# Performance work log

Hardware: AMD Instinct MI355X
Metric: run time of the kernel (lower is better)

## Reference

```python
import jax, jax.numpy as jnp
import numpy as np

B, L, D, H, SPD = 16, 512, 768, 12, 5
DH = D // H
LN_EPS = 1e-5
CLAMP_MIN = 1e-6


def setup_inputs() -> dict:
    key = jax.random.key(0)
    ks = jax.random.split(key, 8)
    s = 1.0 / np.sqrt(D)
    return {
        "tgt": jax.random.normal(ks[0], (B, L, D), jnp.float32),
        "query_pos": jax.random.normal(ks[1], (B, L, D), jnp.float32),
        "pairwise_locs": jax.random.normal(ks[2], (B, L, L, SPD), jnp.float32),
        "Wq": jax.random.normal(ks[3], (D, D), jnp.float32) * s,
        "bq": jnp.zeros((D,), jnp.float32),
        "Wk": jax.random.normal(ks[4], (D, D), jnp.float32) * s,
        "bk": jnp.zeros((D,), jnp.float32),
        "Wv": jax.random.normal(ks[5], (D, D), jnp.float32) * s,
        "bv": jnp.zeros((D,), jnp.float32),
        "Wo": jax.random.normal(ks[6], (D, D), jnp.float32) * s,
        "bo": jnp.zeros((D,), jnp.float32),
        "Wloc": jax.random.normal(ks[7], (SPD, H), jnp.float32) * (1.0 / np.sqrt(SPD)),
        "bloc": jnp.zeros((H,), jnp.float32),
        "ln_g": jnp.ones((D,), jnp.float32),
        "ln_b": jnp.zeros((D,), jnp.float32),
    }


def _layer_norm(x, g, b):
    mu = jnp.mean(x, axis=-1, keepdims=True)
    var = jnp.mean(jnp.square(x - mu), axis=-1, keepdims=True)
    return g * (x - mu) * jax.lax.rsqrt(var + LN_EPS) + b


def reference(tgt, query_pos, pairwise_locs, Wq, bq, Wk, bk, Wv, bv, Wo, bo, Wloc, bloc, ln_g, ln_b):
    # forward_post path: q = k = tgt + query_pos; v = tgt
    qk_in = tgt + query_pos
    q = (qk_in @ Wq + bq).reshape(B, L, H, DH)   # [B,L,H,DH]
    k = (qk_in @ Wk + bk).reshape(B, L, H, DH)
    v = (tgt @ Wv + bv).reshape(B, L, H, DH)

    scale = np.float32(1.0 / np.sqrt(DH))
    attn = jnp.einsum('blhd,bthd->bhlt', q, k) * scale   # [B,H,L,L]

    # spatial fusion 'mul': relu(Linear(pairwise_locs)) -> log-domain additive bias
    loc_attn = jax.nn.relu(pairwise_locs @ Wloc + bloc)   # [B,L,L,H]
    loc_attn = jnp.transpose(loc_attn, (0, 3, 1, 2))      # [B,H,L,L]
    fused = jax.nn.softmax(jnp.log(jnp.clip(loc_attn, CLAMP_MIN, None)) + attn, axis=-1)

    out = jnp.einsum('bhlt,bthd->blhd', fused, v).reshape(B, L, D)
    out = out @ Wo + bo                                   # attn output (tgt2)

    # residual + (dropout p=0) + LayerNorm
    return _layer_norm(tgt + out, ln_g, ln_b)
```

## Files before the change

### kernel.cpp

```cpp
#include <hip/hip_runtime.h>
#include <math.h>

#define BB 16
#define LL 512
#define DD 768
#define HH 12
#define DHH 64
#define SPDD 5
#define MM (BB*LL)
#define LN_EPS 1e-5f
#define CLAMP_MINV 1e-6f

typedef __attribute__((ext_vector_type(8))) short bf8_t;
typedef __attribute__((ext_vector_type(4))) float f4_t;

__device__ __forceinline__ short f2bf(float x) {
    unsigned u = __builtin_bit_cast(unsigned, x);
    unsigned r = (u + 0x7FFFu + ((u >> 16) & 1u)) >> 16;
    return (short)r;
}
__device__ __forceinline__ float bf2f(short s) {
    unsigned u = ((unsigned)(unsigned short)s) << 16;
    return __builtin_bit_cast(float, u);
}

__device__ __forceinline__ void gld16(const short* g, short* l) {
    __builtin_amdgcn_global_load_lds(
        (const __attribute__((address_space(1))) unsigned int*)g,
        (__attribute__((address_space(3))) unsigned int*)l,
        16, 0, 0);
}

__device__ __forceinline__ float block_sum(float v, float* red, int tid) {
    #pragma unroll
    for (int off = 32; off; off >>= 1) v += __shfl_down(v, off, 64);
    __syncthreads();
    if ((tid & 63) == 0) red[tid >> 6] = v;
    __syncthreads();
    return red[0] + red[1] + red[2] + red[3];
}

__global__ __launch_bounds__(256) void wtrans_kernel(
    const float* __restrict__ W0, const float* __restrict__ W1,
    const float* __restrict__ W2, const float* __restrict__ W3,
    short* __restrict__ O0, short* __restrict__ O1,
    short* __restrict__ O2, short* __restrict__ O3)
{
    const float* W; short* O;
    switch (blockIdx.z) {
        case 0: W = W0; O = O0; break;
        case 1: W = W1; O = O1; break;
        case 2: W = W2; O = O2; break;
        default: W = W3; O = O3; break;
    }
    __shared__ float T[64][65];
    const int n0 = blockIdx.x * 64, k0 = blockIdx.y * 64;
    const int tid = threadIdx.x;
    {
        const int kk = tid >> 4, nv = (tid & 15) * 4;
        #pragma unroll
        for (int i = 0; i < 4; ++i) {
            const int k = kk + i * 16;
            const float4 v = *(const float4*)(W + (size_t)(k0 + k) * DD + n0 + nv);
            T[k][nv + 0] = v.x; T[k][nv + 1] = v.y;
            T[k][nv + 2] = v.z; T[k][nv + 3] = v.w;
        }
    }
    __syncthreads();
    {
        const int n = tid >> 2, kc = (tid & 3) * 16;
        short tmp[16];
        #pragma unroll
        for (int i = 0; i < 16; ++i) tmp[i] = f2bf(T[kc + i][n]);
        short* dst = O + (size_t)(n0 + n) * DD + k0 + kc;
        *(bf8_t*)dst       = *(bf8_t*)tmp;
        *(bf8_t*)(dst + 8) = *(bf8_t*)(tmp + 8);
    }
}

__global__ __launch_bounds__(256) void cast_inputs(
    const float* __restrict__ tgt, const float* __restrict__ qpos,
    short* __restrict__ aqk, short* __restrict__ av)
{
    const size_t base = ((size_t)blockIdx.x * 256 + threadIdx.x) * 8;
    const float4 t0 = *(const float4*)(tgt + base);
    const float4 t1 = *(const float4*)(tgt + base + 4);
    const float4 p0 = *(const float4*)(qpos + base);
    const float4 p1 = *(const float4*)(qpos + base + 4);
    short v[8], q[8];
    v[0] = f2bf(t0.x); v[1] = f2bf(t0.y); v[2] = f2bf(t0.z); v[3] = f2bf(t0.w);
    v[4] = f2bf(t1.x); v[5] = f2bf(t1.y); v[6] = f2bf(t1.z); v[7] = f2bf(t1.w);
    q[0] = f2bf(t0.x + p0.x); q[1] = f2bf(t0.y + p0.y);
    q[2] = f2bf(t0.z + p0.z); q[3] = f2bf(t0.w + p0.w);
    q[4] = f2bf(t1.x + p1.x); q[5] = f2bf(t1.y + p1.y);
    q[6] = f2bf(t1.z + p1.z); q[7] = f2bf(t1.w + p1.w);
    *(bf8_t*)(av + base)  = *(bf8_t*)v;
    *(bf8_t*)(aqk + base) = *(bf8_t*)q;
}

__global__ __launch_bounds__(256) void bias_kernel(
    const float* __restrict__ ploc, const float* __restrict__ Wloc,
    const float* __restrict__ bloc, short* __restrict__ out)
{
    const int g   = blockIdx.x * 256 + threadIdx.x;
    const int tch = g & 63;
    const int l   = (g >> 6) & 511;
    const int b   = g >> 15;
    const int t0  = tch * 8;

    float p[40];
    const float* src = ploc + (((size_t)b * LL + l) * LL + t0) * SPDD;
    #pragma unroll
    for (int i = 0; i < 10; ++i)
        *(float4*)(p + i * 4) = *(const float4*)(src + i * 4);

    #pragma unroll
    for (int h = 0; h < HH; ++h) {
        float wl[SPDD];
        #pragma unroll
        for (int s = 0; s < SPDD; ++s) wl[s] = Wloc[s * HH + h];
        const float bl = bloc[h];
        short o[8];
        #pragma unroll
        for (int i = 0; i < 8; ++i) {
            float la = bl;
            #pragma unroll
            for (int s = 0; s < SPDD; ++s) la += p[i * SPDD + s] * wl[s];
            la = fmaxf(fmaxf(la, 0.f), CLAMP_MINV);
            o[i] = f2bf(__logf(la));
        }
        *(bf8_t*)(out + (((size_t)(b * HH + h) * LL + l) * LL + t0)) = *(bf8_t*)o;
    }
}

__global__ __launch_bounds__(256) void gemm_qkv(
    const short* __restrict__ Aqk, const short* __restrict__ Av,
    const short* __restrict__ Wq, const float* __restrict__ bq, short* __restrict__ oq,
    const short* __restrict__ Wk, const float* __restrict__ bk, short* __restrict__ ok,
    const short* __restrict__ Wv, const float* __restrict__ bv, short* __restrict__ ov)
{
    __shared__ short As[128 * 64];
    __shared__ short Bs[128 * 64];
    const int seg = blockIdx.x / 6;
    const int bx = blockIdx.x % 6;
    const int by = blockIdx.y;
    const short* A  = (seg == 2) ? Av : Aqk;
    const short* Wt = (seg == 0) ? Wq : (seg == 1) ? Wk : Wv;
    const float* bias = (seg == 0) ? bq : (seg == 1) ? bk : bv;
    short* out = (seg == 0) ? oq : (seg == 1) ? ok : ov;

    const int n0 = bx * 128, m0 = by * 128;
    const int tid = threadIdx.x;
    const int w = tid >> 6, lane = tid & 63;
    const int quad = lane >> 4, l16 = lane & 15;
    const int wm = w & 1, wn = w >> 1;

    const int sr = w * 8 + (lane >> 3);
    const int sp = lane & 7;

    f4_t acc[4][4];
    #pragma unroll
    for (int i = 0; i < 4; ++i)
        #pragma unroll
        for (int j = 0; j < 4; ++j) acc[i][j] = (f4_t){0.f, 0.f, 0.f, 0.f};

    for (int k0 = 0; k0 < DD; k0 += 64) {
        __syncthreads();
        #pragma unroll
        for (int ra = 0; ra < 4; ++ra) {
            const int r = sr + ra * 32;
            const int c = sp ^ (r & 7);
            const int ldso = ra * 2048 + w * 512 + lane * 8;
            gld16(A  + (size_t)(m0 + r) * DD + k0 + c * 8, As + ldso);
            gld16(Wt + (size_t)(n0 + r) * DD + k0 + c * 8, Bs + ldso);
        }
        __syncthreads();
        #pragma unroll
        for (int s = 0; s < 2; ++s) {
            bf8_t a[4], b[4];
            #pragma unroll
            for (int i = 0; i < 4; ++i) {
                const int rA = wm * 64 + i * 16 + l16;
                const int pA = (s * 4 + quad) ^ (rA & 7);
                a[i] = *(const bf8_t*)(As + rA * 64 + pA * 8);
                const int rB = wn * 64 + i * 16 + l16;
                const int pB = (s * 4 + quad) ^ (rB & 7);
                b[i] = *(const bf8_t*)(Bs + rB * 64 + pB * 8);
            }
            #pragma unroll
            for (int i = 0; i < 4; ++i)
                #pragma unroll
                for (int j = 0; j < 4; ++j)
                    acc[i][j] = __builtin_amdgcn_mfma_f32_16x16x32_bf16(a[i], b[j], acc[i][j], 0, 0, 0);
        }
    }

    float bvv[4];
    #pragma unroll
    for (int j = 0; j < 4; ++j) bvv[j] = bias[n0 + wn * 64 + j * 16 + l16];
    #pragma unroll
    for (int i = 0; i < 4; ++i) {
        #pragma unroll
        for (int j = 0; j < 4; ++j) {
            const int n = n0 + wn * 64 + j * 16 + l16;
            #pragma unroll
            for (int r = 0; r < 4; ++r) {
                const int m = m0 + wm * 64 + i * 16 + quad * 4 + r;
                const float val = acc[i][j][r] + bvv[j];
                const int b_ = m >> 9, l = m & 511;
                const int h = n >> 6, d = n & 63;
                if (seg < 2)
                    out[(((size_t)(b_ * HH + h)) * LL + l) * DHH + d] = f2bf(val);
                else
                    out[(((size_t)(b_ * HH + h)) * DHH + d) * LL + l] = f2bf(val);
            }
        }
    }
}

__global__ __launch_bounds__(256) void gemm_o(
    const short* __restrict__ A, const short* __restrict__ Wt,
    const float* __restrict__ bias, float* __restrict__ out)
{
    __shared__ short As[128 * 64];
    __shared__ short Bs[128 * 64];
    const int bx = blockIdx.x, by = blockIdx.y;
    const int n0 = bx * 128, m0 = by * 128;
    const int tid = threadIdx.x;
    const int w = tid >> 6, lane = tid & 63;
    const int quad = lane >> 4, l16 = lane & 15;
    const int wm = w & 1, wn = w >> 1;
    const int sr = w * 8 + (lane >> 3);
    const int sp = lane & 7;

    f4_t acc[4][4];
    #pragma unroll
    for (int i = 0; i < 4; ++i)
        #pragma unroll
        for (int j = 0; j < 4; ++j) acc[i][j] = (f4_t){0.f, 0.f, 0.f, 0.f};

    for (int k0 = 0; k0 < DD; k0 += 64) {
        __syncthreads();
        #pragma unroll
        for (int ra = 0; ra < 4; ++ra) {
            const int r = sr + ra * 32;
            const int c = sp ^ (r & 7);
            const int ldso = ra * 2048 + w * 512 + lane * 8;
            gld16(A  + (size_t)(m0 + r) * DD + k0 + c * 8, As + ldso);
            gld16(Wt + (size_t)(n0 + r) * DD + k0 + c * 8, Bs + ldso);
        }
        __syncthreads();
        #pragma unroll
        for (int s = 0; s < 2; ++s) {
            bf8_t a[4], b[4];
            #pragma unroll
            for (int i = 0; i < 4; ++i) {
                const int rA = wm * 64 + i * 16 + l16;
                const int pA = (s * 4 + quad) ^ (rA & 7);
                a[i] = *(const bf8_t*)(As + rA * 64 + pA * 8);
                const int rB = wn * 64 + i * 16 + l16;
                const int pB = (s * 4 + quad) ^ (rB & 7);
                b[i] = *(const bf8_t*)(Bs + rB * 64 + pB * 8);
            }
            #pragma unroll
            for (int i = 0; i < 4; ++i)
                #pragma unroll
                for (int j = 0; j < 4; ++j)
                    acc[i][j] = __builtin_amdgcn_mfma_f32_16x16x32_bf16(a[i], b[j], acc[i][j], 0, 0, 0);
        }
    }

    float bvv[4];
    #pragma unroll
    for (int j = 0; j < 4; ++j) bvv[j] = bias[n0 + wn * 64 + j * 16 + l16];
    #pragma unroll
    for (int i = 0; i < 4; ++i)
        #pragma unroll
        for (int j = 0; j < 4; ++j) {
            const int n = n0 + wn * 64 + j * 16 + l16;
            #pragma unroll
            for (int r = 0; r < 4; ++r) {
                const int m = m0 + wm * 64 + i * 16 + quad * 4 + r;
                out[(size_t)m * DD + n] = acc[i][j][r] + bvv[j];
            }
        }
}

template<bool PRE>
__global__ __launch_bounds__(256) void attn_mfma(
    const short* __restrict__ Q, const short* __restrict__ K,
    const short* __restrict__ Vt, const short* __restrict__ LB,
    const float* __restrict__ ploc, const float* __restrict__ Wloc,
    const float* __restrict__ bloc, short* __restrict__ out)
{
    __shared__ short Ks[64 * 64];
    __shared__ short Vs[64 * 64];
    __shared__ short bs16[64 * 68];
    __shared__ short Ps[4][16 * 64];

    const int qt = blockIdx.x, h = blockIdx.y, b = blockIdx.z;
    const int tid = threadIdx.x;
    const int w = tid >> 6, lane = tid & 63;
    const int quad = lane >> 4, l16 = lane & 15;
    const int q0 = qt * 64;
    const size_t bh = (size_t)b * HH + h;

    float wl[SPDD];
    float blc = 0.f;
    if (!PRE) {
        #pragma unroll
        for (int s = 0; s < SPDD; ++s) wl[s] = Wloc[s * HH + h];
        blc = bloc[h];
    }

    const int qr = q0 + w * 16 + l16;
    const bf8_t aq0 = *(const bf8_t*)(Q + (bh * LL + qr) * DHH + quad * 8);
    const bf8_t aq1 = *(const bf8_t*)(Q + (bh * LL + qr) * DHH + quad * 8 + 32);

    f4_t o[4];
    #pragma unroll
    for (int dj = 0; dj < 4; ++dj) o[dj] = (f4_t){0.f, 0.f, 0.f, 0.f};
    float m_row[4], l_row[4];
    #pragma unroll
    for (int r = 0; r < 4; ++r) { m_row[r] = -1e30f; l_row[r] = 0.f; }

    const short* Kg = K  + bh * LL * DHH;
    const short* Vg = Vt + bh * DHH * LL;
    const short* Bg = PRE ? (LB + (bh * LL + q0) * LL) : nullptr;

    const int srow = tid >> 2;
    const int cb   = (tid & 3) * 2;
    const int sw   = srow & 7;

    for (int t0 = 0; t0 < LL; t0 += 64) {
        __syncthreads();
        {
            const short* src = Kg + (size_t)(t0 + srow) * DHH + cb * 8;
            *(bf8_t*)(Ks + srow * 64 + ((cb ^ sw) * 8))       = *(const bf8_t*)(src);
            *(bf8_t*)(Ks + srow * 64 + (((cb + 1) ^ sw) * 8)) = *(const bf8_t*)(src + 8);
        }
        {
            const short* src = Vg + (size_t)srow * LL + t0 + cb * 8;
            *(bf8_t*)(Vs + srow * 64 + ((cb ^ sw) * 8))       = *(const bf8_t*)(src);
            *(bf8_t*)(Vs + srow * 64 + (((cb + 1) ^ sw) * 8)) = *(const bf8_t*)(src + 8);
        }
        {
            const int l = tid >> 2, ts = (tid & 3) * 16;
            if (PRE) {
                const short* src = Bg + (size_t)l * LL + t0 + ts;
                #pragma unroll
                for (int i = 0; i < 4; ++i)
                    *(short4*)(bs16 + l * 68 + ts + i * 4) = *(const short4*)(src + i * 4);
            } else {
                const float* pp = ploc + (((size_t)b * LL + q0 + l) * LL + t0 + ts) * SPDD;
                #pragma unroll
                for (int i = 0; i < 16; ++i) {
                    float la = blc;
                    #pragma unroll
                    for (int s = 0; s < SPDD; ++s) la += pp[i * SPDD + s] * wl[s];
                    la = fmaxf(fmaxf(la, 0.f), CLAMP_MINV);
                    bs16[l * 68 + ts + i] = f2bf(__logf(la));
                }
            }
        }
        __syncthreads();

        f4_t sv[4];
        #pragma unroll
        for (int j = 0; j < 4; ++j) {
            const int rB = j * 16 + l16;
            const int x = rB & 7;
            const bf8_t b0 = *(const bf8_t*)(Ks + rB * 64 + ((quad ^ x) * 8));
            const bf8_t b1 = *(const bf8_t*)(Ks + rB * 64 + (((quad + 4) ^ x) * 8));
            f4_t c = (f4_t){0.f, 0.f, 0.f, 0.f};
            c = __builtin_amdgcn_mfma_f32_16x16x32_bf16(aq0, b0, c, 0, 0, 0);
            c = __builtin_amdgcn_mfma_f32_16x16x32_bf16(aq1, b1, c, 0, 0, 0);
            sv[j] = c;
        }
        #pragma unroll
        for (int j = 0; j < 4; ++j)
            #pragma unroll
            for (int r = 0; r < 4; ++r) {
                const int lrel = w * 16 + quad * 4 + r;
                sv[j][r] = sv[j][r] * 0.125f + bf2f(bs16[lrel * 68 + j * 16 + l16]);
            }
        #pragma unroll
        for (int r = 0; r < 4; ++r) {
            float mx = fmaxf(fmaxf(sv[0][r], sv[1][r]), fmaxf(sv[2][r], sv[3][r]));
            mx = fmaxf(mx, __shfl_xor(mx, 1, 16));
            mx = fmaxf(mx, __shfl_xor(mx, 2, 16));
            mx = fmaxf(mx, __shfl_xor(mx, 4, 16));
            mx = fmaxf(mx, __shfl_xor(mx, 8, 16));
            const float mn = fmaxf(m_row[r], mx);
            const float al = __expf(m_row[r] - mn);
            m_row[r] = mn;
            float rs = 0.f;
            #pragma unroll
            for (int j = 0; j < 4; ++j) {
                const float p = __expf(sv[j][r] - mn);
                sv[j][r] = p;
                rs += p;
            }
            rs += __shfl_xor(rs, 1, 16);
            rs += __shfl_xor(rs, 2, 16);
            rs += __shfl_xor(rs, 4, 16);
            rs += __shfl_xor(rs, 8, 16);
            l_row[r] = l_row[r] * al + rs;
            #pragma unroll
            for (int dj = 0; dj < 4; ++dj) o[dj][r] *= al;
        }
        short* Pw = Ps[w];
        #pragma unroll
        for (int r = 0; r < 4; ++r) {
            const int rp = quad * 4 + r, rp7 = rp & 7;
            #pragma unroll
            for (int j = 0; j < 4; ++j) {
                const int t = j * 16 + l16;
                Pw[rp * 64 + (((t >> 3) ^ rp7) * 8) + (t & 7)] = f2bf(sv[j][r]);
            }
        }
        const int m7 = l16 & 7;
        const bf8_t ap0 = *(const bf8_t*)(Pw + l16 * 64 + ((quad ^ m7) * 8));
        const bf8_t ap1 = *(const bf8_t*)(Pw + l16 * 64 + (((quad + 4) ^ m7) * 8));
        #pragma unroll
        for (int dj = 0; dj < 4; ++dj) {
            const int rB = dj * 16 + l16;
            const int x = rB & 7;
            const bf8_t b0 = *(const bf8_t*)(Vs + rB * 64 + ((quad ^ x) * 8));
            const bf8_t b1 = *(const bf8_t*)(Vs + rB * 64 + (((quad + 4) ^ x) * 8));
            o[dj] = __builtin_amdgcn_mfma_f32_16x16x32_bf16(ap0, b0, o[dj], 0, 0, 0);
            o[dj] = __builtin_amdgcn_mfma_f32_16x16x32_bf16(ap1, b1, o[dj], 0, 0, 0);
        }
    }

    #pragma unroll
    for (int r = 0; r < 4; ++r) {
        const int l = q0 + w * 16 + quad * 4 + r;
        const float inv = 1.f / l_row[r];
        short* op = out + ((size_t)b * LL + l) * DD + h * DHH;
        #pragma unroll
        for (int dj = 0; dj < 4; ++dj)
            op[dj * 16 + l16] = f2bf(o[dj][r] * inv);
    }
}

__global__ __launch_bounds__(256) void ln_kernel(
    const float* __restrict__ x, const float* __restrict__ tgt,
    const float* __restrict__ g, const float* __restrict__ bta,
    float* __restrict__ out)
{
    const int row = blockIdx.x;
    const int tid = threadIdx.x;
    __shared__ float red[4];

    const float* xp = x + (size_t)row * DD;
    const float* tp = tgt + (size_t)row * DD;

    float vals[3];
    float s = 0.f;
    #pragma unroll
    for (int i = 0; i < 3; ++i) {
        const float v = xp[tid + i * 256] + tp[tid + i * 256];
        vals[i] = v;
        s += v;
    }
    s = block_sum(s, red, tid);
    const float mu = s * (1.f / 768.f);

    float vs = 0.f;
    #pragma unroll
    for (int i = 0; i < 3; ++i) {
        const float dv = vals[i] - mu;
        vs += dv * dv;
    }
    vs = block_sum(vs, red, tid);
    const float rstd = rsqrtf(vs * (1.f / 768.f) + LN_EPS);

    #pragma unroll
    for (int i = 0; i < 3; ++i) {
        const int cidx = tid + i * 256;
        out[(size_t)row * DD + cidx] = g[cidx] * (vals[i] - mu) * rstd + bta[cidx];
    }
}

extern "C" void kernel_launch(void* const* d_in, const int* in_sizes, int n_in,
                              void* d_out, int out_size, void* d_ws, size_t ws_size,
                              hipStream_t stream) {
    const float* tgt   = (const float*)d_in[0];
    const float* qpos  = (const float*)d_in[1];
    const float* ploc  = (const float*)d_in[2];
    const float* Wq    = (const float*)d_in[3];
    const float* bq    = (const float*)d_in[4];
    const float* Wk    = (const float*)d_in[5];
    const float* bk    = (const float*)d_in[6];
    const float* Wv    = (const float*)d_in[7];
    const float* bv    = (const float*)d_in[8];
    const float* Wo    = (const float*)d_in[9];
    const float* bo    = (const float*)d_in[10];
    const float* Wloc  = (const float*)d_in[11];
    const float* bloc  = (const float*)d_in[12];
    const float* ln_g  = (const float*)d_in[13];
    const float* ln_b  = (const float*)d_in[14];

    const size_t NQ = (size_t)MM * DD;
    const size_t NW = (size_t)DD * DD;
    const size_t NB = (size_t)BB * HH * LL * LL;

    short* qb   = (short*)d_ws;
    short* kb   = qb  + NQ;
    short* vtb  = kb  + NQ;
    short* aob  = vtb + NQ;
    short* aqk  = aob + NQ;
    short* av   = aqk + NQ;
    float* pbuf = (float*)aqk;
    short* wqt  = av + NQ;
    short* wkt  = wqt + NW;
    short* wvt  = wkt + NW;
    short* wot  = wvt + NW;
    short* lb   = wot + NW;

    const size_t needed = (size_t)(6 * NQ + 4 * NW + NB) * 2;
    const bool pre = (ws_size >= needed);

    wtrans_kernel<<<dim3(12, 12, 4), 256, 0, stream>>>(Wq, Wk, Wv, Wo, wqt, wkt, wvt, wot);
    cast_inputs<<<3072, 256, 0, stream>>>(tgt, qpos, aqk, av);
    if (pre)
        bias_kernel<<<2048, 256, 0, stream>>>(ploc, Wloc, bloc, lb);

    gemm_qkv<<<dim3(18, 64), 256, 0, stream>>>(aqk, av, wqt, bq, qb,
                                               wkt, bk, kb, wvt, bv, vtb);

    if (pre)
        attn_mfma<true ><<<dim3(8, 12, 16), 256, 0, stream>>>(qb, kb, vtb, lb, ploc, Wloc, bloc, aob);
    else
        attn_mfma<false><<<dim3(8, 12, 16), 256, 0, stream>>>(qb, kb, vtb, nullptr, ploc, Wloc, bloc, aob);

    gemm_o<<<dim3(6, 64), 256, 0, stream>>>(aob, wot, bo, pbuf);

    ln_kernel<<<MM, 256, 0, stream>>>(pbuf, tgt, ln_g, ln_b, (float*)d_out);
}
```

Measured before the change: 400.9 us.

## Fuse prep kernels, drop log in favor of multiplicative bias, remap grids for XCD locality

```diff
diff --git a/kernel.cpp b/kernel.cpp
--- a/kernel.cpp
+++ b/kernel.cpp
@@ -40,96 +40,97 @@
     return red[0] + red[1] + red[2] + red[3];
 }
 
-__global__ __launch_bounds__(256) void wtrans_kernel(
+template<bool PRE>
+__global__ __launch_bounds__(256) void prep_kernel(
+    const float* __restrict__ tgt, const float* __restrict__ qpos,
+    const float* __restrict__ ploc, const float* __restrict__ Wloc,
+    const float* __restrict__ bloc,
     const float* __restrict__ W0, const float* __restrict__ W1,
     const float* __restrict__ W2, const float* __restrict__ W3,
+    short* __restrict__ aqk, short* __restrict__ av, short* __restrict__ la,
     short* __restrict__ O0, short* __restrict__ O1,
     short* __restrict__ O2, short* __restrict__ O3)
 {
-    const float* W; short* O;
-    switch (blockIdx.z) {
-        case 0: W = W0; O = O0; break;
-        case 1: W = W1; O = O1; break;
-        case 2: W = W2; O = O2; break;
-        default: W = W3; O = O3; break;
-    }
     __shared__ float T[64][65];
-    const int n0 = blockIdx.x * 64, k0 = blockIdx.y * 64;
-    const int tid = threadIdx.x;
-    {
-        const int kk = tid >> 4, nv = (tid & 15) * 4;
-        #pragma unroll
-        for (int i = 0; i < 4; ++i) {
-            const int k = kk + i * 16;
-            const float4 v = *(const float4*)(W + (size_t)(k0 + k) * DD + n0 + nv);
-            T[k][nv + 0] = v.x; T[k][nv + 1] = v.y;
-            T[k][nv + 2] = v.z; T[k][nv + 3] = v.w;
-        }
-    }
-    __syncthreads();
-    {
-        const int n = tid >> 2, kc = (tid & 3) * 16;
-        short tmp[16];
-        #pragma unroll
-        for (int i = 0; i < 16; ++i) tmp[i] = f2bf(T[kc + i][n]);
-        short* dst = O + (size_t)(n0 + n) * DD + k0 + kc;
-        *(bf8_t*)dst       = *(bf8_t*)tmp;
-        *(bf8_t*)(dst + 8) = *(bf8_t*)(tmp + 8);
-    }
-}
-
-__global__ __launch_bounds__(256) void cast_inputs(
-    const float* __restrict__ tgt, const float* __restrict__ qpos,
-    short* __restrict__ aqk, short* __restrict__ av)
-{
-    const size_t base = ((size_t)blockIdx.x * 256 + threadIdx.x) * 8;
-    const float4 t0 = *(const float4*)(tgt + base);
-    const float4 t1 = *(const float4*)(tgt + base + 4);
-    const float4 p0 = *(const float4*)(qpos + base);
-    const float4 p1 = *(const float4*)(qpos + base + 4);
-    short v[8], q[8];
-    v[0] = f2bf(t0.x); v[1] = f2bf(t0.y); v[2] = f2bf(t0.z); v[3] = f2bf(t0.w);
-    v[4] = f2bf(t1.x); v[5] = f2bf(t1.y); v[6] = f2bf(t1.z); v[7] = f2bf(t1.w);
-    q[0] = f2bf(t0.x + p0.x); q[1] = f2bf(t0.y + p0.y);
-    q[2] = f2bf(t0.z + p0.z); q[3] = f2bf(t0.w + p0.w);
-    q[4] = f2bf(t1.x + p1.x); q[5] = f2bf(t1.y + p1.y);
-    q[6] = f2bf(t1.z + p1.z); q[7] = f2bf(t1.w + p1.w);
-    *(bf8_t*)(av + base)  = *(bf8_t*)v;
-    *(bf8_t*)(aqk + base) = *(bf8_t*)q;
-}
-
-__global__ __launch_bounds__(256) void bias_kernel(
-    const float* __restrict__ ploc, const float* __restrict__ Wloc,
-    const float* __restrict__ bloc, short* __restrict__ out)
-{
-    const int g   = blockIdx.x * 256 + threadIdx.x;
-    const int tch = g & 63;
-    const int l   = (g >> 6) & 511;
-    const int b   = g >> 15;
-    const int t0  = tch * 8;
-
-    float p[40];
-    const float* src = ploc + (((size_t)b * LL + l) * LL + t0) * SPDD;
-    #pragma unroll
-    for (int i = 0; i < 10; ++i)
-        *(float4*)(p + i * 4) = *(const float4*)(src + i * 4);
-
-    #pragma unroll
-    for (int h = 0; h < HH; ++h) {
-        float wl[SPDD];
-        #pragma unroll
-        for (int s = 0; s < SPDD; ++s) wl[s] = Wloc[s * HH + h];
-        const float bl = bloc[h];
-        short o[8];
-        #pragma unroll
-        for (int i = 0; i < 8; ++i) {
-            float la = bl;
-            #pragma unroll
-            for (int s = 0; s < SPDD; ++s) la += p[i * SPDD + s] * wl[s];
-            la = fmaxf(fmaxf(la, 0.f), CLAMP_MINV);
-            o[i] = f2bf(__logf(la));
-        }
-        *(bf8_t*)(out + (((size_t)(b * HH + h) * LL + l) * LL + t0)) = *(bf8_t*)o;
+    const int nbias = PRE ? 2048 : 0;
+    const int t = blockIdx.x;
+    if (PRE && t < nbias) {
+        const int g   = t * 256 + threadIdx.x;
+        const int tch = g & 63;
+        const int l   = (g >> 6) & 511;
+        const int b   = g >> 15;
+        const int t0  = tch * 8;
+        float p[40];
+        const float* src = ploc + (((size_t)b * LL + l) * LL + t0) * SPDD;
+        #pragma unroll
+        for (int i = 0; i < 10; ++i)
+            *(float4*)(p + i * 4) = *(const float4*)(src + i * 4);
+        #pragma unroll
+        for (int h = 0; h < HH; ++h) {
+            float wl[SPDD];
+            #pragma unroll
+            for (int s = 0; s < SPDD; ++s) wl[s] = Wloc[s * HH + h];
+            const float bl = bloc[h];
+            short o[8];
+            #pragma unroll
+            for (int i = 0; i < 8; ++i) {
+                float v = bl;
+                #pragma unroll
+                for (int s = 0; s < SPDD; ++s) v += p[i * SPDD + s] * wl[s];
+                v = fmaxf(fmaxf(v, 0.f), CLAMP_MINV);
+                o[i] = f2bf(v);
+            }
+            *(bf8_t*)(la + (((size_t)(b * HH + h) * LL + l) * LL + t0)) = *(bf8_t*)o;
+        }
+    } else if (t < nbias + 3072) {
+        const int cb = t - nbias;
+        const size_t base = ((size_t)cb * 256 + threadIdx.x) * 8;
+        const float4 t0 = *(const float4*)(tgt + base);
+        const float4 t1 = *(const float4*)(tgt + base + 4);
+        const float4 p0 = *(const float4*)(qpos + base);
+        const float4 p1 = *(const float4*)(qpos + base + 4);
+        short v[8], q[8];
+        v[0] = f2bf(t0.x); v[1] = f2bf(t0.y); v[2] = f2bf(t0.z); v[3] = f2bf(t0.w);
+        v[4] = f2bf(t1.x); v[5] = f2bf(t1.y); v[6] = f2bf(t1.z); v[7] = f2bf(t1.w);
+        q[0] = f2bf(t0.x + p0.x); q[1] = f2bf(t0.y + p0.y);
+        q[2] = f2bf(t0.z + p0.z); q[3] = f2bf(t0.w + p0.w);
+        q[4] = f2bf(t1.x + p1.x); q[5] = f2bf(t1.y + p1.y);
+        q[6] = f2bf(t1.z + p1.z); q[7] = f2bf(t1.w + p1.w);
+        *(bf8_t*)(av + base)  = *(bf8_t*)v;
+        *(bf8_t*)(aqk + base) = *(bf8_t*)q;
+    } else {
+        const int wt = t - (nbias + 3072);
+        const int wi = wt / 144;
+        const int rem = wt % 144;
+        const float* W; short* O;
+        switch (wi) {
+            case 0: W = W0; O = O0; break;
+            case 1: W = W1; O = O1; break;
+            case 2: W = W2; O = O2; break;
+            default: W = W3; O = O3; break;
+        }
+        const int n0 = (rem % 12) * 64, k0 = (rem / 12) * 64;
+        const int tid = threadIdx.x;
+        {
+            const int kk = tid >> 4, nv = (tid & 15) * 4;
+            #pragma unroll
+            for (int i = 0; i < 4; ++i) {
+                const int k = kk + i * 16;
+                const float4 v = *(const float4*)(W + (size_t)(k0 + k) * DD + n0 + nv);
+                T[k][nv + 0] = v.x; T[k][nv + 1] = v.y;
+                T[k][nv + 2] = v.z; T[k][nv + 3] = v.w;
+            }
+        }
+        __syncthreads();
+        {
+            const int n = tid >> 2, kc = (tid & 3) * 16;
+            short tmp[16];
+            #pragma unroll
+            for (int i = 0; i < 16; ++i) tmp[i] = f2bf(T[kc + i][n]);
+            short* dst = O + (size_t)(n0 + n) * DD + k0 + kc;
+            *(bf8_t*)dst       = *(bf8_t*)tmp;
+            *(bf8_t*)(dst + 8) = *(bf8_t*)(tmp + 8);
+        }
     }
 }
 
@@ -141,9 +142,12 @@
 {
     __shared__ short As[128 * 64];
     __shared__ short Bs[128 * 64];
-    const int seg = blockIdx.x / 6;
-    const int bx = blockIdx.x % 6;
-    const int by = blockIdx.y;
+    const int id = blockIdx.y * 18 + blockIdx.x;
+    const int xcd = id & 7, j = id >> 3;
+    const int by = xcd * 8 + j / 18;
+    const int gx = j % 18;
+    const int seg = gx / 6;
+    const int bx = gx % 6;
     const short* A  = (seg == 2) ? Av : Aqk;
     const short* Wt = (seg == 0) ? Wq : (seg == 1) ? Wk : Wv;
     const float* bias = (seg == 0) ? bq : (seg == 1) ? bk : bv;
@@ -154,7 +158,6 @@
     const int w = tid >> 6, lane = tid & 63;
     const int quad = lane >> 4, l16 = lane & 15;
     const int wm = w & 1, wn = w >> 1;
-
     const int sr = w * 8 + (lane >> 3);
     const int sp = lane & 7;
 
@@ -162,7 +165,7 @@
     #pragma unroll
     for (int i = 0; i < 4; ++i)
         #pragma unroll
-        for (int j = 0; j < 4; ++j) acc[i][j] = (f4_t){0.f, 0.f, 0.f, 0.f};
+        for (int jj = 0; jj < 4; ++jj) acc[i][jj] = (f4_t){0.f, 0.f, 0.f, 0.f};
 
     for (int k0 = 0; k0 < DD; k0 += 64) {
         __syncthreads();
@@ -190,23 +193,23 @@
             #pragma unroll
             for (int i = 0; i < 4; ++i)
                 #pragma unroll
-                for (int j = 0; j < 4; ++j)
-                    acc[i][j] = __builtin_amdgcn_mfma_f32_16x16x32_bf16(a[i], b[j], acc[i][j], 0, 0, 0);
+                for (int jj = 0; jj < 4; ++jj)
+                    acc[i][jj] = __builtin_amdgcn_mfma_f32_16x16x32_bf16(a[i], b[jj], acc[i][jj], 0, 0, 0);
         }
     }
 
     float bvv[4];
     #pragma unroll
-    for (int j = 0; j < 4; ++j) bvv[j] = bias[n0 + wn * 64 + j * 16 + l16];
+    for (int jj = 0; jj < 4; ++jj) bvv[jj] = bias[n0 + wn * 64 + jj * 16 + l16];
     #pragma unroll
     for (int i = 0; i < 4; ++i) {
         #pragma unroll
-        for (int j = 0; j < 4; ++j) {
-            const int n = n0 + wn * 64 + j * 16 + l16;
+        for (int jj = 0; jj < 4; ++jj) {
+            const int n = n0 + wn * 64 + jj * 16 + l16;
             #pragma unroll
             for (int r = 0; r < 4; ++r) {
                 const int m = m0 + wm * 64 + i * 16 + quad * 4 + r;
-                const float val = acc[i][j][r] + bvv[j];
+                const float val = acc[i][jj][r] + bvv[jj];
                 const int b_ = m >> 9, l = m & 511;
                 const int h = n >> 6, d = n & 63;
                 if (seg < 2)
@@ -224,7 +227,10 @@
 {
     __shared__ short As[128 * 64];
     __shared__ short Bs[128 * 64];
-    const int bx = blockIdx.x, by = blockIdx.y;
+    const int id = blockIdx.y * 6 + blockIdx.x;
+    const int xcd = id & 7, j = id >> 3;
+    const int by = xcd * 8 + j / 6;
+    const int bx = j % 6;
     const int n0 = bx * 128, m0 = by * 128;
     const int tid = threadIdx.x;
     const int w = tid >> 6, lane = tid & 63;
@@ -237,7 +243,7 @@
     #pragma unroll
     for (int i = 0; i < 4; ++i)
         #pragma unroll
-        for (int j = 0; j < 4; ++j) acc[i][j] = (f4_t){0.f, 0.f, 0.f, 0.f};
+        for (int jj = 0; jj < 4; ++jj) acc[i][jj] = (f4_t){0.f, 0.f, 0.f, 0.f};
 
     for (int k0 = 0; k0 < DD; k0 += 64) {
         __syncthreads();
@@ -265,23 +271,23 @@
             #pragma unroll
             for (int i = 0; i < 4; ++i)
                 #pragma unroll
-                for (int j = 0; j < 4; ++j)
-                    acc[i][j] = __builtin_amdgcn_mfma_f32_16x16x32_bf16(a[i], b[j], acc[i][j], 0, 0, 0);
+                for (int jj = 0; jj < 4; ++jj)
+                    acc[i][jj] = __builtin_amdgcn_mfma_f32_16x16x32_bf16(a[i], b[jj], acc[i][jj], 0, 0, 0);
         }
     }
 
     float bvv[4];
     #pragma unroll
-    for (int j = 0; j < 4; ++j) bvv[j] = bias[n0 + wn * 64 + j * 16 + l16];
+    for (int jj = 0; jj < 4; ++jj) bvv[jj] = bias[n0 + wn * 64 + jj * 16 + l16];
     #pragma unroll
     for (int i = 0; i < 4; ++i)
         #pragma unroll
-        for (int j = 0; j < 4; ++j) {
-            const int n = n0 + wn * 64 + j * 16 + l16;
+        for (int jj = 0; jj < 4; ++jj) {
+            const int n = n0 + wn * 64 + jj * 16 + l16;
             #pragma unroll
             for (int r = 0; r < 4; ++r) {
                 const int m = m0 + wm * 64 + i * 16 + quad * 4 + r;
-                out[(size_t)m * DD + n] = acc[i][j][r] + bvv[j];
+                out[(size_t)m * DD + n] = acc[i][jj][r] + bvv[jj];
             }
         }
 }
@@ -289,7 +295,7 @@
 template<bool PRE>
 __global__ __launch_bounds__(256) void attn_mfma(
     const short* __restrict__ Q, const short* __restrict__ K,
-    const short* __restrict__ Vt, const short* __restrict__ LB,
+    const short* __restrict__ Vt, const short* __restrict__ LA,
     const float* __restrict__ ploc, const float* __restrict__ Wloc,
     const float* __restrict__ bloc, short* __restrict__ out)
 {
@@ -298,7 +304,8 @@
     __shared__ short bs16[64 * 68];
     __shared__ short Ps[4][16 * 64];
 
-    const int qt = blockIdx.x, h = blockIdx.y, b = blockIdx.z;
+    const int h = blockIdx.x % 12, b = blockIdx.x / 12;
+    const int qt = blockIdx.y;
     const int tid = threadIdx.x;
     const int w = tid >> 6, lane = tid & 63;
     const int quad = lane >> 4, l16 = lane & 15;
@@ -326,7 +333,7 @@
 
     const short* Kg = K  + bh * LL * DHH;
     const short* Vg = Vt + bh * DHH * LL;
-    const short* Bg = PRE ? (LB + (bh * LL + q0) * LL) : nullptr;
+    const short* Bg = PRE ? (LA + (bh * LL + q0) * LL) : nullptr;
 
     const int srow = tid >> 2;
     const int cb   = (tid & 3) * 2;
@@ -355,11 +362,11 @@
                 const float* pp = ploc + (((size_t)b * LL + q0 + l) * LL + t0 + ts) * SPDD;
                 #pragma unroll
                 for (int i = 0; i < 16; ++i) {
-                    float la = blc;
+                    float v = blc;
                     #pragma unroll
-                    for (int s = 0; s < SPDD; ++s) la += pp[i * SPDD + s] * wl[s];
-                    la = fmaxf(fmaxf(la, 0.f), CLAMP_MINV);
-                    bs16[l * 68 + ts + i] = f2bf(__logf(la));
+                    for (int s = 0; s < SPDD; ++s) v += pp[i * SPDD + s] * wl[s];
+                    v = fmaxf(fmaxf(v, 0.f), CLAMP_MINV);
+                    bs16[l * 68 + ts + i] = f2bf(v);
                 }
             }
         }
@@ -380,12 +387,11 @@
         #pragma unroll
         for (int j = 0; j < 4; ++j)
             #pragma unroll
-            for (int r = 0; r < 4; ++r) {
-                const int lrel = w * 16 + quad * 4 + r;
-                sv[j][r] = sv[j][r] * 0.125f + bf2f(bs16[lrel * 68 + j * 16 + l16]);
-            }
+            for (int r = 0; r < 4; ++r) sv[j][r] *= 0.125f;
+
         #pragma unroll
         for (int r = 0; r < 4; ++r) {
+            const int lrel = w * 16 + quad * 4 + r;
             float mx = fmaxf(fmaxf(sv[0][r], sv[1][r]), fmaxf(sv[2][r], sv[3][r]));
             mx = fmaxf(mx, __shfl_xor(mx, 1, 16));
             mx = fmaxf(mx, __shfl_xor(mx, 2, 16));
@@ -397,7 +403,8 @@
             float rs = 0.f;
             #pragma unroll
             for (int j = 0; j < 4; ++j) {
-                const float p = __expf(sv[j][r] - mn);
+                const float lav = bf2f(bs16[lrel * 68 + j * 16 + l16]);
+                const float p = lav * __expf(sv[j][r] - mn);
                 sv[j][r] = p;
                 rs += p;
             }
@@ -517,23 +524,27 @@
     short* wkt  = wqt + NW;
     short* wvt  = wkt + NW;
     short* wot  = wvt + NW;
-    short* lb   = wot + NW;
+    short* lab  = wot + NW;
 
     const size_t needed = (size_t)(6 * NQ + 4 * NW + NB) * 2;
     const bool pre = (ws_size >= needed);
 
-    wtrans_kernel<<<dim3(12, 12, 4), 256, 0, stream>>>(Wq, Wk, Wv, Wo, wqt, wkt, wvt, wot);
-    cast_inputs<<<3072, 256, 0, stream>>>(tgt, qpos, aqk, av);
     if (pre)
-        bias_kernel<<<2048, 256, 0, stream>>>(ploc, Wloc, bloc, lb);
+        prep_kernel<true ><<<5696, 256, 0, stream>>>(tgt, qpos, ploc, Wloc, bloc,
+                                                     Wq, Wk, Wv, Wo,
+                                                     aqk, av, lab, wqt, wkt, wvt, wot);
+    else
+        prep_kernel<false><<<3648, 256, 0, stream>>>(tgt, qpos, ploc, Wloc, bloc,
+                                                     Wq, Wk, Wv, Wo,
+                                                     aqk, av, lab, wqt, wkt, wvt, wot);
 
     gemm_qkv<<<dim3(18, 64), 256, 0, stream>>>(aqk, av, wqt, bq, qb,
                                                wkt, bk, kb, wvt, bv, vtb);
 
     if (pre)
-        attn_mfma<true ><<<dim3(8, 12, 16), 256, 0, stream>>>(qb, kb, vtb, lb, ploc, Wloc, bloc, aob);
+        attn_mfma<true ><<<dim3(192, 8), 256, 0, stream>>>(qb, kb, vtb, lab, ploc, Wloc, bloc, aob);
     else
-        attn_mfma<false><<<dim3(8, 12, 16), 256, 0, stream>>>(qb, kb, vtb, nullptr, ploc, Wloc, bloc, aob);
+        attn_mfma<false><<<dim3(192, 8), 256, 0, stream>>>(qb, kb, vtb, nullptr, ploc, Wloc, bloc, aob);
 
     gemm_o<<<dim3(6, 64), 256, 0, stream>>>(aob, wot, bo, pbuf);
 
```

After: 368.4 us. 8.1% less time.
